# Kernel optimization log

Measured on AMD Instinct MI355X. Metric: run time of the kernel, lower is better.

The kernel has to match this reference:

```python
import jax, jax.numpy as jnp
import numpy as np

B = 4096
N0 = 784          # MNIST input
L0 = 263          # fc0: Gather chain 784 -> 256 (ELU after each)
L2 = 121          # fc2: Gather chain 256 -> 12 (ELU after each); final Gather 12 -> 10 has no ELU


def _win3(x):
    # x: (B, N) -> (B, N-2, 3) sliding windows of width 3
    return jnp.stack([x[:, :-2], x[:, 1:-1], x[:, 2:]], axis=-1)


def setup_inputs() -> dict:
    key = jax.random.key(0)
    kx, k0, k1, k2, k3, k4 = jax.random.split(key, 6)
    s = 0.75  # keeps activation variance roughly stable through ~380 ELU glia layers
    x = jax.random.normal(kx, (B, N0), jnp.float32)
    W0 = jax.random.normal(k0, (L0, 782, 3), jnp.float32) * s
    m0 = np.arange(782)[None, :] < (780 - 2 * np.arange(L0))[:, None]
    W0 = W0 * jnp.asarray(m0[..., None], jnp.float32)  # zero out rows past each layer's out size
    Ws = jax.random.normal(k1, (256, 3), jnp.float32) * s
    bs = jax.random.normal(k2, (256,), jnp.float32) * 0.1
    W2 = jax.random.normal(k3, (L2, 254, 3), jnp.float32) * s
    m2 = np.arange(254)[None, :] < (252 - 2 * np.arange(L2))[:, None]
    W2 = W2 * jnp.asarray(m2[..., None], jnp.float32)
    Wlast = jax.random.normal(k4, (10, 3), jnp.float32) * s
    return {"x": x, "W0": W0, "Ws": Ws, "bs": bs, "W2": W2, "Wlast": Wlast}


def reference(x, W0, Ws, bs, W2, Wlast):
    def gather_step(h, W):
        # locally-connected width-3 Gather (out = in - 2, bias=False) + ELU.
        # Invalid tail rows of W are zero, so padded positions stay exactly 0
        # (ELU(0)=0) and never contaminate valid windows.
        y = jax.nn.elu(jnp.einsum('bjk,jk->bj', _win3(h), W))
        return jnp.pad(y, ((0, 0), (0, 2))), None

    # fc0: 263 Gather+ELU layers, 784 -> 256 (valid prefix of fixed-width state)
    h, _ = jax.lax.scan(gather_step, x, W0)
    h = h[:, :256]
    # fc1: Slide(256) + ELU -- same-size width-3 locally connected layer, zero-padded window, bias
    hp = jnp.pad(h, ((0, 0), (1, 1)))
    h = jax.nn.elu(jnp.einsum('bjk,jk->bj', _win3(hp), Ws) + bs)
    # fc2: 121 Gather+ELU layers, 256 -> 12
    h, _ = jax.lax.scan(gather_step, h, W2)
    # final Gather(12): 12 -> 10, no ELU
    logits = jnp.einsum('bjk,jk->bj', _win3(h[:, :12]), Wlast)
    return jax.nn.log_softmax(logits, axis=1)
```

## Files before the change

### kernel.cpp

```cpp
#include <hip/hip_runtime.h>
#include <math.h>


#define G 2

#define T_TOTAL 580864

__device__ __forceinline__ float elu_f(float a) {
    return a > 0.0f ? a : (__expf(a) - 1.0f);
}

template<int N>
__device__ __forceinline__ void load_w(float (&w)[N], const float* __restrict__ p) {
#pragma unroll
    for (int j = 0; j < N; ++j) w[j] = p[j];
}

template<int K, int NW>
__device__ __forceinline__ void scan_layer(float (&h)[K], const float (&w)[NW]) {
    static_assert(NW >= 3 * K, "weight array too small");
    float e0 = __shfl_down(h[0], 1);
    float e1;
    if constexpr (K >= 2) e1 = __shfl_down(h[1], 1);
    else                  e1 = __shfl_down(h[0], 2);
#pragma unroll
    for (int i = 0; i < K; ++i) {
        float x1 = (i + 1 < K) ? h[i + 1] : e0;
        float x2 = (i + 2 < K) ? h[i + 2] : ((i + 2 == K) ? e0 : e1);
        float a = fmaf(h[i], w[3 * i], fmaf(x1, w[3 * i + 1], x2 * w[3 * i + 2]));
        h[i] = elu_f(a);
    }
}

template<int NC, int NW>
__device__ __forceinline__ void load_wt(float (&w)[NW], const float4* __restrict__ Tp, int lr) {
#pragma unroll
    for (int c = 0; c < NC; ++c) {
        float4 v = Tp[(size_t)lr * (NC * 64) + c * 64];
        w[4 * c + 0] = v.x; w[4 * c + 1] = v.y; w[4 * c + 2] = v.z; w[4 * c + 3] = v.w;
    }
}

template<int K, int NC>
__device__ __forceinline__ void scan_phase_t(const float* __restrict__ Tphase, int nl,
                                             int lane, float (&hA)[K], float (&hB)[K]) {
    const float4* __restrict__ Tp = reinterpret_cast<const float4*>(Tphase) + lane;
    float wa[4 * NC], wb[4 * NC];
    load_wt<NC>(wa, Tp, 0);
    int l = 0;
    for (; l + 2 <= nl; l += 2) {
        load_wt<NC>(wb, Tp, l + 1);
        scan_layer<K>(hA, wa);
        scan_layer<K>(hB, wa);
        if (l + 3 <= nl) load_wt<NC>(wa, Tp, l + 2);
        scan_layer<K>(hA, wb);
        scan_layer<K>(hB, wb);
    }
    if (l < nl) { scan_layer<K>(hA, wa); scan_layer<K>(hB, wa); }
}

template<int K>
__device__ __forceinline__ void scan_phase(const float* __restrict__ W, int lstride,
                                           int l0, int l1, int lane,
                                           float (&hA)[K], float (&hB)[K]) {
    int base = 3 * K * lane;
    if (base + 3 * K > lstride) base = lstride - 3 * K;
    const float* __restrict__ Wp = W + (size_t)l0 * lstride + base;
    float wa[3 * K], wb[3 * K];
    load_w(wa, Wp);
    int l = l0;
    for (; l + 2 <= l1; l += 2) {
        load_w(wb, Wp + lstride);
        scan_layer<K>(hA, wa);
        scan_layer<K>(hB, wa);
        if (l + 3 <= l1) load_w(wa, Wp + 2 * (size_t)lstride);
        scan_layer<K>(hA, wb);
        scan_layer<K>(hB, wb);
        Wp += 2 * (size_t)lstride;
    }
    if (l < l1) { scan_layer<K>(hA, wa); scan_layer<K>(hB, wa); }
}

template<int KA, int KB>
__device__ __forceinline__ void repack2(float (&aA)[KA], float (&aB)[KA],
                                        float (&nA)[KB], float (&nB)[KB],
                                        float* lds, int lane) {
    __syncthreads();
#pragma unroll
    for (int i = 0; i < KA; ++i) lds[KA * lane + i] = aA[i];
    __syncthreads();
#pragma unroll
    for (int i = 0; i < KB; ++i) nA[i] = lds[KB * lane + i];
    __syncthreads();
#pragma unroll
    for (int i = 0; i < KA; ++i) lds[KA * lane + i] = aB[i];
    __syncthreads();
#pragma unroll
    for (int i = 0; i < KB; ++i) nB[i] = lds[KB * lane + i];
    __syncthreads();
}

__device__ __forceinline__ void stage2(float (&hA)[5], float (&hB)[5],
                                       const float* __restrict__ Ws,
                                       const float* __restrict__ bs, int lane) {
#pragma unroll
    for (int i = 0; i < 5; ++i) {
        if (5 * lane + i > 255) { hA[i] = 0.0f; hB[i] = 0.0f; }
    }
    float w[15], bb[5];
#pragma unroll
    for (int i = 0; i < 5; ++i) {
        int j = 5 * lane + i;
        bool v = j < 256;
        w[3 * i + 0] = v ? Ws[3 * j + 0] : 0.0f;
        w[3 * i + 1] = v ? Ws[3 * j + 1] : 0.0f;
        w[3 * i + 2] = v ? Ws[3 * j + 2] : 0.0f;
        bb[i]        = v ? bs[j]         : 0.0f;
    }
    float pA = __shfl_up(hA[4], 1); if (lane == 0) pA = 0.0f;
    float pB = __shfl_up(hB[4], 1); if (lane == 0) pB = 0.0f;
    float qA = __shfl_down(hA[0], 1);
    float qB = __shfl_down(hB[0], 1);
    float yA[5], yB[5];
#pragma unroll
    for (int i = 0; i < 5; ++i) {
        float xmA = (i == 0) ? pA : hA[i - 1];
        float xpA = (i == 4) ? qA : hA[i + 1];
        yA[i] = elu_f(fmaf(xmA, w[3 * i], fmaf(hA[i], w[3 * i + 1], fmaf(xpA, w[3 * i + 2], bb[i]))));
        float xmB = (i == 0) ? pB : hB[i - 1];
        float xpB = (i == 4) ? qB : hB[i + 1];
        yB[i] = elu_f(fmaf(xmB, w[3 * i], fmaf(hB[i], w[3 * i + 1], fmaf(xpB, w[3 * i + 2], bb[i]))));
    }
#pragma unroll
    for (int i = 0; i < 5; ++i) { hA[i] = yA[i]; hB[i] = yB[i]; }
}

__device__ __forceinline__ void emit_row(float v, const float* __restrict__ Wl,
                                         float* __restrict__ out, int row, int lane) {
    float n1 = __shfl_down(v, 1);
    float n2 = __shfl_down(v, 2);
    float lg = 0.0f;
    if (lane < 10)
        lg = fmaf(v, Wl[3 * lane], fmaf(n1, Wl[3 * lane + 1], n2 * Wl[3 * lane + 2]));
    float t = (lane < 10) ? lg : -1e30f;
#pragma unroll
    for (int d = 1; d < 16; d <<= 1) t = fmaxf(t, __shfl_xor(t, d));
    float e = (lane < 10) ? __expf(lg - t) : 0.0f;
    float s = e;
#pragma unroll
    for (int d = 1; d < 16; d <<= 1) s += __shfl_xor(s, d);
    float lse = t + __logf(s);
    if (lane < 10) out[(size_t)row * 10 + lane] = lg - lse;
}

__global__ __launch_bounds__(256)
void reorder_w(const float* __restrict__ W0, const float* __restrict__ W2,
               float* __restrict__ T) {
    int idx = blockIdx.x * 256 + threadIdx.x;
    if (idx >= T_TOTAL) return;
    int base, l0, K, NC, lstride; const float* Wsrc;
    if      (idx < 181760) { base = 0;      l0 = 0;   K = 13; NC = 10; Wsrc = W0; lstride = 2346; }
    else if (idx < 378368) { base = 181760; l0 = 71;  K = 10; NC = 8;  Wsrc = W0; lstride = 2346; }
    else if (idx < 476672) { base = 378368; l0 = 167; K = 7;  NC = 6;  Wsrc = W0; lstride = 2346; }
    else if (idx < 509440) { base = 476672; l0 = 231; K = 5;  NC = 4;  Wsrc = W0; lstride = 2346; }
    else if (idx < 533248) { base = 509440; l0 = 0;   K = 4;  NC = 3;  Wsrc = W2; lstride = 762;  }
    else if (idx < 557824) { base = 533248; l0 = 31;  K = 3;  NC = 3;  Wsrc = W2; lstride = 762;  }
    else if (idx < 574208) { base = 557824; l0 = 63;  K = 2;  NC = 2;  Wsrc = W2; lstride = 762;  }
    else                   { base = 574208; l0 = 95;  K = 1;  NC = 1;  Wsrc = W2; lstride = 762;  }
    int rel  = idx - base;
    int perL = NC * 256;
    int lr   = rel / perL;
    int r2   = rel - lr * perL;
    int c    = r2 >> 8;
    int ln   = (r2 >> 2) & 63;
    int f    = r2 & 3;
    int elem = 4 * c + f;
    float v = 0.0f;
    if (elem < 3 * K) {
        int b = 3 * K * ln;
        if (b + 3 * K > lstride) b = lstride - 3 * K;
        v = Wsrc[(size_t)(l0 + lr) * lstride + b + elem];
    }
    T[idx] = v;
}

__global__ __launch_bounds__(64)
void pg_kernel_t(const float* __restrict__ x,  const float* __restrict__ Ws,
                 const float* __restrict__ bs, const float* __restrict__ Wlast,
                 const float* __restrict__ T,  float* __restrict__ out)
{
    __shared__ float lds[13 * 64];
    const int lane = threadIdx.x;
    const int rowA = blockIdx.x * G;
    const int rowB = rowA + 1;

    float a13[13], b13[13];
#pragma unroll
    for (int i = 0; i < 13; ++i) {
        int p = 13 * lane + i;
        a13[i] = (p < 784) ? x[(size_t)rowA * 784 + p] : 0.0f;
        b13[i] = (p < 784) ? x[(size_t)rowB * 784 + p] : 0.0f;
    }

    scan_phase_t<13, 10>(T + 0,      71, lane, a13, b13);
    float a10[10], b10[10]; repack2<13, 10>(a13, b13, a10, b10, lds, lane);
    scan_phase_t<10, 8>(T + 181760,  96, lane, a10, b10);
    float a7[7], b7[7];     repack2<10, 7>(a10, b10, a7, b7, lds, lane);
    scan_phase_t<7, 6>(T + 378368,   64, lane, a7, b7);
    float a5[5], b5[5];     repack2<7, 5>(a7, b7, a5, b5, lds, lane);
    scan_phase_t<5, 4>(T + 476672,   32, lane, a5, b5);

    stage2(a5, b5, Ws, bs, lane);

    float a4[4], b4[4];     repack2<5, 4>(a5, b5, a4, b4, lds, lane);
    scan_phase_t<4, 3>(T + 509440,   31, lane, a4, b4);
    float a3[3], b3[3];     repack2<4, 3>(a4, b4, a3, b3, lds, lane);
    scan_phase_t<3, 3>(T + 533248,   32, lane, a3, b3);
    float a2_[2], b2_[2];   repack2<3, 2>(a3, b3, a2_, b2_, lds, lane);
    scan_phase_t<2, 2>(T + 557824,   32, lane, a2_, b2_);
    float a1[1], b1[1];     repack2<2, 1>(a2_, b2_, a1, b1, lds, lane);
    scan_phase_t<1, 1>(T + 574208,   26, lane, a1, b1);

    emit_row(a1[0], Wlast, out, rowA, lane);
    emit_row(b1[0], Wlast, out, rowB, lane);
}

__global__ __launch_bounds__(64)
void pg_kernel_d(const float* __restrict__ x,  const float* __restrict__ W0,
                 const float* __restrict__ Ws, const float* __restrict__ bs,
                 const float* __restrict__ W2, const float* __restrict__ Wlast,
                 float* __restrict__ out)
{
    __shared__ float lds[13 * 64];
    const int lane = threadIdx.x;
    const int rowA = blockIdx.x * G;
    const int rowB = rowA + 1;

    float a13[13], b13[13];
#pragma unroll
    for (int i = 0; i < 13; ++i) {
        int p = 13 * lane + i;
        a13[i] = (p < 784) ? x[(size_t)rowA * 784 + p] : 0.0f;
        b13[i] = (p < 784) ? x[(size_t)rowB * 784 + p] : 0.0f;
    }

    scan_phase<13>(W0, 2346, 0, 71, lane, a13, b13);
    float a10[10], b10[10]; repack2<13, 10>(a13, b13, a10, b10, lds, lane);
    scan_phase<10>(W0, 2346, 71, 167, lane, a10, b10);
    float a7[7], b7[7];     repack2<10, 7>(a10, b10, a7, b7, lds, lane);
    scan_phase<7>(W0, 2346, 167, 231, lane, a7, b7);
    float a5[5], b5[5];     repack2<7, 5>(a7, b7, a5, b5, lds, lane);
    scan_phase<5>(W0, 2346, 231, 263, lane, a5, b5);

    stage2(a5, b5, Ws, bs, lane);

    float a4[4], b4[4];     repack2<5, 4>(a5, b5, a4, b4, lds, lane);
    scan_phase<4>(W2, 762, 0, 31, lane, a4, b4);
    float a3[3], b3[3];     repack2<4, 3>(a4, b4, a3, b3, lds, lane);
    scan_phase<3>(W2, 762, 31, 63, lane, a3, b3);
    float a2_[2], b2_[2];   repack2<3, 2>(a3, b3, a2_, b2_, lds, lane);
    scan_phase<2>(W2, 762, 63, 95, lane, a2_, b2_);
    float a1[1], b1[1];     repack2<2, 1>(a2_, b2_, a1, b1, lds, lane);
    scan_phase<1>(W2, 762, 95, 121, lane, a1, b1);

    emit_row(a1[0], Wlast, out, rowA, lane);
    emit_row(b1[0], Wlast, out, rowB, lane);
}

extern "C" void kernel_launch(void* const* d_in, const int* in_sizes, int n_in,
                              void* d_out, int out_size, void* d_ws, size_t ws_size,
                              hipStream_t stream) {
    const float* x     = (const float*)d_in[0];
    const float* W0    = (const float*)d_in[1];
    const float* Ws    = (const float*)d_in[2];
    const float* bs    = (const float*)d_in[3];
    const float* W2    = (const float*)d_in[4];
    const float* Wlast = (const float*)d_in[5];
    float* out = (float*)d_out;

    if (ws_size >= (size_t)T_TOTAL * sizeof(float)) {
        float* T = (float*)d_ws;
        reorder_w<<<(T_TOTAL + 255) / 256, 256, 0, stream>>>(W0, W2, T);
        pg_kernel_t<<<4096 / G, 64, 0, stream>>>(x, Ws, bs, Wlast, T, out);
    } else {
        pg_kernel_d<<<4096 / G, 64, 0, stream>>>(x, W0, Ws, bs, W2, Wlast, out);
    }
}
```

Baseline: 258.9 us.

## Pack two batch rows into float2 with packed FMA and finer repack phases

The main kernel now keeps the two batch rows per wave as float2 pairs and computes each layer with inline-asm v_pk_mul_f32/v_pk_fma_f32, broadcasting one weight across both rows through op_sel. ELU uses a packed multiply by log2(e) followed by v_exp_f32. fc0 is split into nine phases instead of four, so each lane's register width shrinks by one every ~32 layers. That drops padding work, and the reorder table is rebuilt with the new phase boundaries. The cost is more LDS repacks with syncs and hand-written asm that bypasses compiler scheduling.

```diff
diff --git a/kernel.cpp b/kernel.cpp
--- a/kernel.cpp
+++ b/kernel.cpp
@@ -4,135 +4,144 @@
 
 #define G 2
 
-#define T_TOTAL 580864
+template<int HI>
+__device__ __forceinline__ float2 pk_mul_b(float2 a, float2 w) {
+    float2 d;
+    if constexpr (HI)
+        asm("v_pk_mul_f32 %0, %1, %2 op_sel:[0,1] op_sel_hi:[1,1]"
+            : "=v"(d) : "v"(a), "v"(w));
+    else
+        asm("v_pk_mul_f32 %0, %1, %2 op_sel_hi:[1,0]"
+            : "=v"(d) : "v"(a), "v"(w));
+    return d;
+}
+template<int HI>
+__device__ __forceinline__ float2 pk_fma_b(float2 a, float2 w, float2 c) {
+    float2 d;
+    if constexpr (HI)
+        asm("v_pk_fma_f32 %0, %1, %2, %3 op_sel:[0,1,0] op_sel_hi:[1,1,1]"
+            : "=v"(d) : "v"(a), "v"(w), "v"(c));
+    else
+        asm("v_pk_fma_f32 %0, %1, %2, %3 op_sel_hi:[1,0,1]"
+            : "=v"(d) : "v"(a), "v"(w), "v"(c));
+    return d;
+}
+__device__ __forceinline__ float2 pk_mul2(float2 a, float2 b) {
+    float2 d;
+    asm("v_pk_mul_f32 %0, %1, %2" : "=v"(d) : "v"(a), "v"(b));
+    return d;
+}
+__device__ __forceinline__ float vexp2(float x) {
+    float d;
+    asm("v_exp_f32 %0, %1" : "=v"(d) : "v"(x));
+    return d;
+}
 
 __device__ __forceinline__ float elu_f(float a) {
     return a > 0.0f ? a : (__expf(a) - 1.0f);
 }
 
-template<int N>
-__device__ __forceinline__ void load_w(float (&w)[N], const float* __restrict__ p) {
-#pragma unroll
-    for (int j = 0; j < N; ++j) w[j] = p[j];
+template<int K, int I, int NW>
+__device__ __forceinline__ void slot_run(float2 (&h)[K], const float2 (&w)[NW],
+                                         float2 e0, float2 e1, float2 l2e) {
+    if constexpr (I < K) {
+        float2 x1, x2;
+        if constexpr (I + 1 < K) x1 = h[I + 1]; else x1 = e0;
+        if constexpr (I + 2 < K) x2 = h[I + 2];
+        else if constexpr (I + 2 == K) x2 = e0;
+        else x2 = e1;
+        float2 acc = pk_mul_b<(3 * I + 2) & 1>(x2, w[(3 * I + 2) >> 1]);
+        acc = pk_fma_b<(3 * I + 1) & 1>(x1, w[(3 * I + 1) >> 1], acc);
+        acc = pk_fma_b<(3 * I) & 1>(h[I], w[(3 * I) >> 1], acc);
+        float2 t = pk_mul2(acc, l2e);
+        float ex = vexp2(t.x) - 1.0f;
+        float ey = vexp2(t.y) - 1.0f;
+        h[I].x = acc.x > 0.0f ? acc.x : ex;
+        h[I].y = acc.y > 0.0f ? acc.y : ey;
+        slot_run<K, I + 1, NW>(h, w, e0, e1, l2e);
+    }
 }
 
 template<int K, int NW>
-__device__ __forceinline__ void scan_layer(float (&h)[K], const float (&w)[NW]) {
-    static_assert(NW >= 3 * K, "weight array too small");
-    float e0 = __shfl_down(h[0], 1);
-    float e1;
-    if constexpr (K >= 2) e1 = __shfl_down(h[1], 1);
-    else                  e1 = __shfl_down(h[0], 2);
-#pragma unroll
-    for (int i = 0; i < K; ++i) {
-        float x1 = (i + 1 < K) ? h[i + 1] : e0;
-        float x2 = (i + 2 < K) ? h[i + 2] : ((i + 2 == K) ? e0 : e1);
-        float a = fmaf(h[i], w[3 * i], fmaf(x1, w[3 * i + 1], x2 * w[3 * i + 2]));
-        h[i] = elu_f(a);
-    }
-}
-
-template<int NC, int NW>
-__device__ __forceinline__ void load_wt(float (&w)[NW], const float4* __restrict__ Tp, int lr) {
+__device__ __forceinline__ void scan_layer_pk(float2 (&h)[K], const float2 (&w)[NW],
+                                              float2 l2e) {
+    float2 e0, e1;
+    e0.x = __shfl_down(h[0].x, 1); e0.y = __shfl_down(h[0].y, 1);
+    if constexpr (K >= 2) { e1.x = __shfl_down(h[1].x, 1); e1.y = __shfl_down(h[1].y, 1); }
+    else                  { e1.x = __shfl_down(h[0].x, 2); e1.y = __shfl_down(h[0].y, 2); }
+    slot_run<K, 0, NW>(h, w, e0, e1, l2e);
+}
+
+template<int NC>
+__device__ __forceinline__ void load_wt2(float2 (&w)[2 * NC], const float4* __restrict__ Tp,
+                                         int lr) {
 #pragma unroll
     for (int c = 0; c < NC; ++c) {
         float4 v = Tp[(size_t)lr * (NC * 64) + c * 64];
-        w[4 * c + 0] = v.x; w[4 * c + 1] = v.y; w[4 * c + 2] = v.z; w[4 * c + 3] = v.w;
+        w[2 * c]     = make_float2(v.x, v.y);
+        w[2 * c + 1] = make_float2(v.z, v.w);
     }
 }
 
 template<int K, int NC>
-__device__ __forceinline__ void scan_phase_t(const float* __restrict__ Tphase, int nl,
-                                             int lane, float (&hA)[K], float (&hB)[K]) {
+__device__ __forceinline__ void scan_phase_pk(const float* __restrict__ Tphase, int nl,
+                                              int lane, float2 (&h)[K], float2 l2e) {
     const float4* __restrict__ Tp = reinterpret_cast<const float4*>(Tphase) + lane;
-    float wa[4 * NC], wb[4 * NC];
-    load_wt<NC>(wa, Tp, 0);
+    float2 wa[2 * NC], wb[2 * NC];
+    load_wt2<NC>(wa, Tp, 0);
     int l = 0;
     for (; l + 2 <= nl; l += 2) {
-        load_wt<NC>(wb, Tp, l + 1);
-        scan_layer<K>(hA, wa);
-        scan_layer<K>(hB, wa);
-        if (l + 3 <= nl) load_wt<NC>(wa, Tp, l + 2);
-        scan_layer<K>(hA, wb);
-        scan_layer<K>(hB, wb);
-    }
-    if (l < nl) { scan_layer<K>(hA, wa); scan_layer<K>(hB, wa); }
-}
-
-template<int K>
-__device__ __forceinline__ void scan_phase(const float* __restrict__ W, int lstride,
-                                           int l0, int l1, int lane,
-                                           float (&hA)[K], float (&hB)[K]) {
-    int base = 3 * K * lane;
-    if (base + 3 * K > lstride) base = lstride - 3 * K;
-    const float* __restrict__ Wp = W + (size_t)l0 * lstride + base;
-    float wa[3 * K], wb[3 * K];
-    load_w(wa, Wp);
-    int l = l0;
-    for (; l + 2 <= l1; l += 2) {
-        load_w(wb, Wp + lstride);
-        scan_layer<K>(hA, wa);
-        scan_layer<K>(hB, wa);
-        if (l + 3 <= l1) load_w(wa, Wp + 2 * (size_t)lstride);
-        scan_layer<K>(hA, wb);
-        scan_layer<K>(hB, wb);
-        Wp += 2 * (size_t)lstride;
-    }
-    if (l < l1) { scan_layer<K>(hA, wa); scan_layer<K>(hB, wa); }
+        load_wt2<NC>(wb, Tp, l + 1);
+        scan_layer_pk<K>(h, wa, l2e);
+        if (l + 3 <= nl) load_wt2<NC>(wa, Tp, l + 2);
+        scan_layer_pk<K>(h, wb, l2e);
+    }
+    if (l < nl) scan_layer_pk<K>(h, wa, l2e);
 }
 
 template<int KA, int KB>
-__device__ __forceinline__ void repack2(float (&aA)[KA], float (&aB)[KA],
-                                        float (&nA)[KB], float (&nB)[KB],
-                                        float* lds, int lane) {
-    __syncthreads();
-#pragma unroll
-    for (int i = 0; i < KA; ++i) lds[KA * lane + i] = aA[i];
-    __syncthreads();
-#pragma unroll
-    for (int i = 0; i < KB; ++i) nA[i] = lds[KB * lane + i];
-    __syncthreads();
-#pragma unroll
-    for (int i = 0; i < KA; ++i) lds[KA * lane + i] = aB[i];
-    __syncthreads();
-#pragma unroll
-    for (int i = 0; i < KB; ++i) nB[i] = lds[KB * lane + i];
-    __syncthreads();
-}
-
-__device__ __forceinline__ void stage2(float (&hA)[5], float (&hB)[5],
-                                       const float* __restrict__ Ws,
-                                       const float* __restrict__ bs, int lane) {
-#pragma unroll
-    for (int i = 0; i < 5; ++i) {
-        if (5 * lane + i > 255) { hA[i] = 0.0f; hB[i] = 0.0f; }
-    }
-    float w[15], bb[5];
+__device__ __forceinline__ void repack_pk(float2 (&a)[KA], float2 (&n)[KB],
+                                          float2* lds, int lane) {
+    __syncthreads();
+#pragma unroll
+    for (int i = 0; i < KA; ++i) lds[KA * lane + i] = a[i];
+    __syncthreads();
+#pragma unroll
+    for (int i = 0; i < KB; ++i) n[i] = lds[KB * lane + i];
+    __syncthreads();
+}
+
+__device__ __forceinline__ void stage2_pk(float2 (&h)[5], const float* __restrict__ Ws,
+                                          const float* __restrict__ bs, int lane) {
+#pragma unroll
+    for (int i = 0; i < 5; ++i)
+        if (5 * lane + i > 255) h[i] = make_float2(0.f, 0.f);
+    float w0[5], w1[5], w2[5], bb[5];
 #pragma unroll
     for (int i = 0; i < 5; ++i) {
         int j = 5 * lane + i;
         bool v = j < 256;
-        w[3 * i + 0] = v ? Ws[3 * j + 0] : 0.0f;
-        w[3 * i + 1] = v ? Ws[3 * j + 1] : 0.0f;
-        w[3 * i + 2] = v ? Ws[3 * j + 2] : 0.0f;
-        bb[i]        = v ? bs[j]         : 0.0f;
-    }
-    float pA = __shfl_up(hA[4], 1); if (lane == 0) pA = 0.0f;
-    float pB = __shfl_up(hB[4], 1); if (lane == 0) pB = 0.0f;
-    float qA = __shfl_down(hA[0], 1);
-    float qB = __shfl_down(hB[0], 1);
-    float yA[5], yB[5];
+        w0[i] = v ? Ws[3 * j + 0] : 0.f;
+        w1[i] = v ? Ws[3 * j + 1] : 0.f;
+        w2[i] = v ? Ws[3 * j + 2] : 0.f;
+        bb[i] = v ? bs[j] : 0.f;
+    }
+    float2 p, q;
+    p.x = __shfl_up(h[4].x, 1); p.y = __shfl_up(h[4].y, 1);
+    if (lane == 0) p = make_float2(0.f, 0.f);
+    q.x = __shfl_down(h[0].x, 1); q.y = __shfl_down(h[0].y, 1);
+    float2 y[5];
 #pragma unroll
     for (int i = 0; i < 5; ++i) {
-        float xmA = (i == 0) ? pA : hA[i - 1];
-        float xpA = (i == 4) ? qA : hA[i + 1];
-        yA[i] = elu_f(fmaf(xmA, w[3 * i], fmaf(hA[i], w[3 * i + 1], fmaf(xpA, w[3 * i + 2], bb[i]))));
-        float xmB = (i == 0) ? pB : hB[i - 1];
-        float xpB = (i == 4) ? qB : hB[i + 1];
-        yB[i] = elu_f(fmaf(xmB, w[3 * i], fmaf(hB[i], w[3 * i + 1], fmaf(xpB, w[3 * i + 2], bb[i]))));
-    }
-#pragma unroll
-    for (int i = 0; i < 5; ++i) { hA[i] = yA[i]; hB[i] = yB[i]; }
+        float2 xm = (i == 0) ? p : h[i - 1];
+        float2 xp = (i == 4) ? q : h[i + 1];
+        float ax = fmaf(xm.x, w0[i], fmaf(h[i].x, w1[i], fmaf(xp.x, w2[i], bb[i])));
+        float ay = fmaf(xm.y, w0[i], fmaf(h[i].y, w1[i], fmaf(xp.y, w2[i], bb[i])));
+        y[i].x = elu_f(ax);
+        y[i].y = elu_f(ay);
+    }
+#pragma unroll
+    for (int i = 0; i < 5; ++i) h[i] = y[i];
 }
 
 __device__ __forceinline__ void emit_row(float v, const float* __restrict__ Wl,
@@ -153,20 +162,29 @@
     if (lane < 10) out[(size_t)row * 10 + lane] = lg - lse;
 }
 
+#define T_TOTAL 531712
+
 __global__ __launch_bounds__(256)
 void reorder_w(const float* __restrict__ W0, const float* __restrict__ W2,
                float* __restrict__ T) {
     int idx = blockIdx.x * 256 + threadIdx.x;
     if (idx >= T_TOTAL) return;
-    int base, l0, K, NC, lstride; const float* Wsrc;
-    if      (idx < 181760) { base = 0;      l0 = 0;   K = 13; NC = 10; Wsrc = W0; lstride = 2346; }
-    else if (idx < 378368) { base = 181760; l0 = 71;  K = 10; NC = 8;  Wsrc = W0; lstride = 2346; }
-    else if (idx < 476672) { base = 378368; l0 = 167; K = 7;  NC = 6;  Wsrc = W0; lstride = 2346; }
-    else if (idx < 509440) { base = 476672; l0 = 231; K = 5;  NC = 4;  Wsrc = W0; lstride = 2346; }
-    else if (idx < 533248) { base = 509440; l0 = 0;   K = 4;  NC = 3;  Wsrc = W2; lstride = 762;  }
-    else if (idx < 557824) { base = 533248; l0 = 31;  K = 3;  NC = 3;  Wsrc = W2; lstride = 762;  }
-    else if (idx < 574208) { base = 557824; l0 = 63;  K = 2;  NC = 2;  Wsrc = W2; lstride = 762;  }
-    else                   { base = 574208; l0 = 95;  K = 1;  NC = 1;  Wsrc = W2; lstride = 762;  }
+    int base, l0, K, NC, s1;
+    if      (idx < 17920)  { base = 0;      l0 = 0;   K = 13; NC = 10; s1 = 1; }
+    else if (idx < 91648)  { base = 17920;  l0 = 7;   K = 12; NC = 9;  s1 = 1; }
+    else if (idx < 165376) { base = 91648;  l0 = 39;  K = 11; NC = 9;  s1 = 1; }
+    else if (idx < 230912) { base = 165376; l0 = 71;  K = 10; NC = 8;  s1 = 1; }
+    else if (idx < 288256) { base = 230912; l0 = 103; K = 9;  NC = 7;  s1 = 1; }
+    else if (idx < 337408) { base = 288256; l0 = 135; K = 8;  NC = 6;  s1 = 1; }
+    else if (idx < 386560) { base = 337408; l0 = 167; K = 7;  NC = 6;  s1 = 1; }
+    else if (idx < 427520) { base = 386560; l0 = 199; K = 6;  NC = 5;  s1 = 1; }
+    else if (idx < 460288) { base = 427520; l0 = 231; K = 5;  NC = 4;  s1 = 1; }
+    else if (idx < 484096) { base = 460288; l0 = 0;   K = 4;  NC = 3;  s1 = 0; }
+    else if (idx < 508672) { base = 484096; l0 = 31;  K = 3;  NC = 3;  s1 = 0; }
+    else if (idx < 525056) { base = 508672; l0 = 63;  K = 2;  NC = 2;  s1 = 0; }
+    else                   { base = 525056; l0 = 95;  K = 1;  NC = 1;  s1 = 0; }
+    const float* Wsrc = s1 ? W0 : W2;
+    int lstride = s1 ? 2346 : 762;
     int rel  = idx - base;
     int perL = NC * 256;
     int lr   = rel / perL;
@@ -185,46 +203,105 @@
 }
 
 __global__ __launch_bounds__(64)
-void pg_kernel_t(const float* __restrict__ x,  const float* __restrict__ Ws,
-                 const float* __restrict__ bs, const float* __restrict__ Wlast,
-                 const float* __restrict__ T,  float* __restrict__ out)
+void pg_kernel_pk(const float* __restrict__ x,  const float* __restrict__ Ws,
+                  const float* __restrict__ bs, const float* __restrict__ Wlast,
+                  const float* __restrict__ T,  float* __restrict__ out)
 {
-    __shared__ float lds[13 * 64];
+    __shared__ float2 lds2[13 * 64];
     const int lane = threadIdx.x;
     const int rowA = blockIdx.x * G;
     const int rowB = rowA + 1;
-
-    float a13[13], b13[13];
+    const float2 l2e = make_float2(1.44269504088896340736f, 1.44269504088896340736f);
+
+    float2 h13[13];
 #pragma unroll
     for (int i = 0; i < 13; ++i) {
         int p = 13 * lane + i;
-        a13[i] = (p < 784) ? x[(size_t)rowA * 784 + p] : 0.0f;
-        b13[i] = (p < 784) ? x[(size_t)rowB * 784 + p] : 0.0f;
-    }
-
-    scan_phase_t<13, 10>(T + 0,      71, lane, a13, b13);
-    float a10[10], b10[10]; repack2<13, 10>(a13, b13, a10, b10, lds, lane);
-    scan_phase_t<10, 8>(T + 181760,  96, lane, a10, b10);
-    float a7[7], b7[7];     repack2<10, 7>(a10, b10, a7, b7, lds, lane);
-    scan_phase_t<7, 6>(T + 378368,   64, lane, a7, b7);
-    float a5[5], b5[5];     repack2<7, 5>(a7, b7, a5, b5, lds, lane);
-    scan_phase_t<5, 4>(T + 476672,   32, lane, a5, b5);
-
-    stage2(a5, b5, Ws, bs, lane);
-
-    float a4[4], b4[4];     repack2<5, 4>(a5, b5, a4, b4, lds, lane);
-    scan_phase_t<4, 3>(T + 509440,   31, lane, a4, b4);
-    float a3[3], b3[3];     repack2<4, 3>(a4, b4, a3, b3, lds, lane);
-    scan_phase_t<3, 3>(T + 533248,   32, lane, a3, b3);
-    float a2_[2], b2_[2];   repack2<3, 2>(a3, b3, a2_, b2_, lds, lane);
-    scan_phase_t<2, 2>(T + 557824,   32, lane, a2_, b2_);
-    float a1[1], b1[1];     repack2<2, 1>(a2_, b2_, a1, b1, lds, lane);
-    scan_phase_t<1, 1>(T + 574208,   26, lane, a1, b1);
-
-    emit_row(a1[0], Wlast, out, rowA, lane);
-    emit_row(b1[0], Wlast, out, rowB, lane);
-}
-
+        h13[i].x = (p < 784) ? x[(size_t)rowA * 784 + p] : 0.0f;
+        h13[i].y = (p < 784) ? x[(size_t)rowB * 784 + p] : 0.0f;
+    }
+
+    scan_phase_pk<13, 10>(T + 0,      7,  lane, h13, l2e);
+    float2 h12[12]; repack_pk<13, 12>(h13, h12, lds2, lane);
+    scan_phase_pk<12, 9>(T + 17920,   32, lane, h12, l2e);
+    float2 h11[11]; repack_pk<12, 11>(h12, h11, lds2, lane);
+    scan_phase_pk<11, 9>(T + 91648,   32, lane, h11, l2e);
+    float2 h10[10]; repack_pk<11, 10>(h11, h10, lds2, lane);
+    scan_phase_pk<10, 8>(T + 165376,  32, lane, h10, l2e);
+    float2 h9[9];   repack_pk<10, 9>(h10, h9, lds2, lane);
+    scan_phase_pk<9, 7>(T + 230912,   32, lane, h9, l2e);
+    float2 h8[8];   repack_pk<9, 8>(h9, h8, lds2, lane);
+    scan_phase_pk<8, 6>(T + 288256,   32, lane, h8, l2e);
+    float2 h7[7];   repack_pk<8, 7>(h8, h7, lds2, lane);
+    scan_phase_pk<7, 6>(T + 337408,   32, lane, h7, l2e);
+    float2 h6[6];   repack_pk<7, 6>(h7, h6, lds2, lane);
+    scan_phase_pk<6, 5>(T + 386560,   32, lane, h6, l2e);
+    float2 h5[5];   repack_pk<6, 5>(h6, h5, lds2, lane);
+    scan_phase_pk<5, 4>(T + 427520,   32, lane, h5, l2e);
+
+    stage2_pk(h5, Ws, bs, lane);
+
+    float2 h4[4];   repack_pk<5, 4>(h5, h4, lds2, lane);
+    scan_phase_pk<4, 3>(T + 460288,   31, lane, h4, l2e);
+    float2 h3[3];   repack_pk<4, 3>(h4, h3, lds2, lane);
+    scan_phase_pk<3, 3>(T + 484096,   32, lane, h3, l2e);
+    float2 h2[2];   repack_pk<3, 2>(h3, h2, lds2, lane);
+    scan_phase_pk<2, 2>(T + 508672,   32, lane, h2, l2e);
+    float2 h1[1];   repack_pk<2, 1>(h2, h1, lds2, lane);
+    scan_phase_pk<1, 1>(T + 525056,   26, lane, h1, l2e);
+
+    emit_row(h1[0].x, Wlast, out, rowA, lane);
+    emit_row(h1[0].y, Wlast, out, rowB, lane);
+}
+
+template<int K>
+__device__ __forceinline__ void scan_layer_s(float (&h)[K], const float (&w)[3 * K]) {
+    float e0 = __shfl_down(h[0], 1);
+    float e1;
+    if constexpr (K >= 2) e1 = __shfl_down(h[1], 1);
+    else                  e1 = __shfl_down(h[0], 2);
+#pragma unroll
+    for (int i = 0; i < K; ++i) {
+        float x1 = (i + 1 < K) ? h[i + 1] : e0;
+        float x2 = (i + 2 < K) ? h[i + 2] : ((i + 2 == K) ? e0 : e1);
+        float a = fmaf(h[i], w[3 * i], fmaf(x1, w[3 * i + 1], x2 * w[3 * i + 2]));
+        h[i] = elu_f(a);
+    }
+}
+template<int K>
+__device__ __forceinline__ void scan_phase_s(const float* __restrict__ W, int lstride,
+                                             int l0, int l1, int lane,
+                                             float (&hA)[K], float (&hB)[K]) {
+    int base = 3 * K * lane;
+    if (base + 3 * K > lstride) base = lstride - 3 * K;
+    const float* __restrict__ Wp = W + (size_t)l0 * lstride + base;
+    float wa[3 * K];
+    for (int l = l0; l < l1; ++l) {
+#pragma unroll
+        for (int j = 0; j < 3 * K; ++j) wa[j] = Wp[j];
+        scan_layer_s<K>(hA, wa);
+        scan_layer_s<K>(hB, wa);
+        Wp += lstride;
+    }
+}
+template<int KA, int KB>
+__device__ __forceinline__ void repack_s(float (&aA)[KA], float (&aB)[KA],
+                                         float (&nA)[KB], float (&nB)[KB],
+                                         float* lds, int lane) {
+    __syncthreads();
+#pragma unroll
+    for (int i = 0; i < KA; ++i) lds[KA * lane + i] = aA[i];
+    __syncthreads();
+#pragma unroll
+    for (int i = 0; i < KB; ++i) nA[i] = lds[KB * lane + i];
+    __syncthreads();
+#pragma unroll
+    for (int i = 0; i < KA; ++i) lds[KA * lane + i] = aB[i];
+    __syncthreads();
+#pragma unroll
+    for (int i = 0; i < KB; ++i) nB[i] = lds[KB * lane + i];
+    __syncthreads();
+}
 __global__ __launch_bounds__(64)
 void pg_kernel_d(const float* __restrict__ x,  const float* __restrict__ W0,
                  const float* __restrict__ Ws, const float* __restrict__ bs,
@@ -235,7 +312,6 @@
     const int lane = threadIdx.x;
     const int rowA = blockIdx.x * G;
     const int rowB = rowA + 1;
-
     float a13[13], b13[13];
 #pragma unroll
     for (int i = 0; i < 13; ++i) {
@@ -243,26 +319,29 @@
         a13[i] = (p < 784) ? x[(size_t)rowA * 784 + p] : 0.0f;
         b13[i] = (p < 784) ? x[(size_t)rowB * 784 + p] : 0.0f;
     }
-
-    scan_phase<13>(W0, 2346, 0, 71, lane, a13, b13);
-    float a10[10], b10[10]; repack2<13, 10>(a13, b13, a10, b10, lds, lane);
-    scan_phase<10>(W0, 2346, 71, 167, lane, a10, b10);
-    float a7[7], b7[7];     repack2<10, 7>(a10, b10, a7, b7, lds, lane);
-    scan_phase<7>(W0, 2346, 167, 231, lane, a7, b7);
-    float a5[5], b5[5];     repack2<7, 5>(a7, b7, a5, b5, lds, lane);
-    scan_phase<5>(W0, 2346, 231, 263, lane, a5, b5);
-
-    stage2(a5, b5, Ws, bs, lane);
-
-    float a4[4], b4[4];     repack2<5, 4>(a5, b5, a4, b4, lds, lane);
-    scan_phase<4>(W2, 762, 0, 31, lane, a4, b4);
-    float a3[3], b3[3];     repack2<4, 3>(a4, b4, a3, b3, lds, lane);
-    scan_phase<3>(W2, 762, 31, 63, lane, a3, b3);
-    float a2_[2], b2_[2];   repack2<3, 2>(a3, b3, a2_, b2_, lds, lane);
-    scan_phase<2>(W2, 762, 63, 95, lane, a2_, b2_);
-    float a1[1], b1[1];     repack2<2, 1>(a2_, b2_, a1, b1, lds, lane);
-    scan_phase<1>(W2, 762, 95, 121, lane, a1, b1);
-
+    scan_phase_s<13>(W0, 2346, 0, 71, lane, a13, b13);
+    float a10[10], b10[10]; repack_s<13, 10>(a13, b13, a10, b10, lds, lane);
+    scan_phase_s<10>(W0, 2346, 71, 167, lane, a10, b10);
+    float a7[7], b7[7];     repack_s<10, 7>(a10, b10, a7, b7, lds, lane);
+    scan_phase_s<7>(W0, 2346, 167, 231, lane, a7, b7);
+    float a5[5], b5[5];     repack_s<7, 5>(a7, b7, a5, b5, lds, lane);
+    scan_phase_s<5>(W0, 2346, 231, 263, lane, a5, b5);
+    {
+        float2 hp[5];
+#pragma unroll
+        for (int i = 0; i < 5; ++i) hp[i] = make_float2(a5[i], b5[i]);
+        stage2_pk(hp, Ws, bs, lane);
+#pragma unroll
+        for (int i = 0; i < 5; ++i) { a5[i] = hp[i].x; b5[i] = hp[i].y; }
+    }
+    float a4[4], b4[4];     repack_s<5, 4>(a5, b5, a4, b4, lds, lane);
+    scan_phase_s<4>(W2, 762, 0, 31, lane, a4, b4);
+    float a3[3], b3[3];     repack_s<4, 3>(a4, b4, a3, b3, lds, lane);
+    scan_phase_s<3>(W2, 762, 31, 63, lane, a3, b3);
+    float a2_[2], b2_[2];   repack_s<3, 2>(a3, b3, a2_, b2_, lds, lane);
+    scan_phase_s<2>(W2, 762, 63, 95, lane, a2_, b2_);
+    float a1[1], b1[1];     repack_s<2, 1>(a2_, b2_, a1, b1, lds, lane);
+    scan_phase_s<1>(W2, 762, 95, 121, lane, a1, b1);
     emit_row(a1[0], Wlast, out, rowA, lane);
     emit_row(b1[0], Wlast, out, rowB, lane);
 }
@@ -281,7 +360,7 @@
     if (ws_size >= (size_t)T_TOTAL * sizeof(float)) {
         float* T = (float*)d_ws;
         reorder_w<<<(T_TOTAL + 255) / 256, 256, 0, stream>>>(W0, W2, T);
-        pg_kernel_t<<<4096 / G, 64, 0, stream>>>(x, Ws, bs, Wlast, T, out);
+        pg_kernel_pk<<<4096 / G, 64, 0, stream>>>(x, Ws, bs, Wlast, T, out);
     } else {
         pg_kernel_d<<<4096 / G, 64, 0, stream>>>(x, W0, Ws, bs, W2, Wlast, out);
     }
```

Result: faster. 245.6 us (-5.1%).
